# Performance work log

Measured on AMD Instinct MI355X. Metric: run time of the kernel, lower is better.

## Reference

```python
import jax, jax.numpy as jnp
import numpy as np

N, E = 50000, 300000
IN_C, HID, OUT_C, HEADS = 256, 64, 128, 4
HW = HID * HEADS  # 256


def gat_conv(x, edge_index, W, att_src, att_dst, bias, concat):
    # x: [N, F_in], W: [F_in, H*C], att_*: [H, C], edge_index: [2, E] (src -> dst)
    H, C = att_src.shape
    n = x.shape[0]
    src, dst = edge_index[0], edge_index[1]
    h = (x @ W).reshape(n, H, C)                      # [N, H, C]
    a_src = jnp.einsum('nhc,hc->nh', h, att_src)      # [N, H]
    a_dst = jnp.einsum('nhc,hc->nh', h, att_dst)      # [N, H]
    e = jax.nn.leaky_relu(a_src[src] + a_dst[dst], 0.2)  # [E, H]
    m = jax.ops.segment_max(e, dst, num_segments=n)   # per-dst max for stable softmax
    m = jnp.where(jnp.isfinite(m), m, 0.0)
    ex = jnp.exp(e - m[dst])                          # [E, H]
    denom = jax.ops.segment_sum(ex, dst, num_segments=n)
    alpha = ex / (denom[dst] + 1e-16)                 # [E, H]
    msg = h[src] * alpha[:, :, None]                  # [E, H, C]
    out = jax.ops.segment_sum(msg, dst, num_segments=n)  # [N, H, C]
    if concat:
        return out.reshape(n, H * C) + bias
    return out.mean(axis=1) + bias


def setup_inputs() -> dict:
    key = jax.random.key(0)
    ks = jax.random.split(key, 24)
    inp = {}
    inp['x'] = jax.random.normal(ks[0], (N, IN_C), dtype=jnp.float32)
    inp['edge_index'] = jax.random.randint(ks[1], (2, E), 0, N, dtype=jnp.int32)
    def glorot(k, shape):
        fan = shape[0] + shape[-1]
        return jax.random.uniform(k, shape, jnp.float32, -1.0, 1.0) * np.sqrt(6.0 / fan)
    # layer 0: GATConv(256 -> 64, heads=4, concat) + Linear(256 -> 256)
    inp['W0'] = glorot(ks[2], (IN_C, HW)); inp['as0'] = glorot(ks[3], (HEADS, HID)); inp['ad0'] = glorot(ks[4], (HEADS, HID)); inp['b0'] = jnp.zeros((HW,), jnp.float32)
    inp['lw0'] = glorot(ks[5], (IN_C, HW)); inp['lb0'] = jnp.zeros((HW,), jnp.float32)
    # layer 1: GATConv(256 -> 64, heads=4, concat) + Linear(256 -> 256)
    inp['W1'] = glorot(ks[6], (HW, HW)); inp['as1'] = glorot(ks[7], (HEADS, HID)); inp['ad1'] = glorot(ks[8], (HEADS, HID)); inp['b1'] = jnp.zeros((HW,), jnp.float32)
    inp['lw1'] = glorot(ks[9], (HW, HW)); inp['lb1'] = jnp.zeros((HW,), jnp.float32)
    # layer 2: GATConv(256 -> 128, heads=4, concat=False mean) + Linear(256 -> 128)
    inp['W2'] = glorot(ks[10], (HW, HEADS * OUT_C)); inp['as2'] = glorot(ks[11], (HEADS, OUT_C)); inp['ad2'] = glorot(ks[12], (HEADS, OUT_C)); inp['b2'] = jnp.zeros((OUT_C,), jnp.float32)
    inp['lw2'] = glorot(ks[13], (HW, OUT_C)); inp['lb2'] = jnp.zeros((OUT_C,), jnp.float32)
    return inp


def reference(x, edge_index, W0, as0, ad0, b0, lw0, lb0, W1, as1, ad1, b1, lw1, lb1, W2, as2, ad2, b2, lw2, lb2):
    # layer 0
    h = gat_conv(x, edge_index, W0, as0, ad0, b0, concat=True) + (x @ lw0 + lb0)
    h = jax.nn.elu(h)  # dropout p=0.0 -> identity
    # layer 1
    h = gat_conv(h, edge_index, W1, as1, ad1, b1, concat=True) + (h @ lw1 + lb1)
    h = jax.nn.elu(h)
    # layer 2 (no activation)
    out = gat_conv(h, edge_index, W2, as2, ad2, b2, concat=False) + (h @ lw2 + lb2)
    return out
```

## Files before the change

### kernel.cpp

```cpp
#include <hip/hip_runtime.h>
#include <cstddef>


typedef __bf16 bf16x8 __attribute__((ext_vector_type(8)));
typedef float floatx4 __attribute__((ext_vector_type(4)));
typedef unsigned short ushortx8 __attribute__((ext_vector_type(8)));

__device__ __forceinline__ unsigned short bf16_rn(float f) {
    unsigned int u = __float_as_uint(f);
    u += 0x7FFF + ((u >> 16) & 1);
    return (unsigned short)(u >> 16);
}
__device__ __forceinline__ float bf16_tof(unsigned short h) {
    return __uint_as_float(((unsigned int)h) << 16);
}

__device__ __forceinline__ float amax_decode(unsigned int u) {
    unsigned int bits = (u >> 31) ? (u & 0x7FFFFFFFu) : ~u;
    return __uint_as_float(bits);
}

__device__ __forceinline__ void gload_lds16(const void* g, void* l) {
    __builtin_amdgcn_global_load_lds(
        (const __attribute__((address_space(1))) unsigned int*)g,
        (__attribute__((address_space(3))) unsigned int*)l, 16, 0, 0);
}


__global__ __launch_bounds__(1024) void scan_kernel(const int* __restrict__ deg,
                                                    int* __restrict__ off, int n) {
    __shared__ int wsum[16];
    __shared__ int carry_s;
    int tid = threadIdx.x, lane = tid & 63, wid = tid >> 6;
    if (tid == 0) { carry_s = 0; off[0] = 0; }
    __syncthreads();
    for (int base = 0; base < n; base += 1024) {
        int i = base + tid;
        int v = (i < n) ? deg[i] : 0;
        int s = v;
        #pragma unroll
        for (int d = 1; d < 64; d <<= 1) {
            int t = __shfl_up(s, d, 64);
            if (lane >= d) s += t;
        }
        if (lane == 63) wsum[wid] = s;
        __syncthreads();
        if (wid == 0) {
            int wv = (lane < 16) ? wsum[lane] : 0;
            #pragma unroll
            for (int d = 1; d < 16; d <<= 1) {
                int t = __shfl_up(wv, d, 64);
                if (lane >= d) wv += t;
            }
            if (lane < 16) wsum[lane] = wv;
        }
        __syncthreads();
        int prev = (wid > 0) ? wsum[wid - 1] : 0;
        int inc = carry_s + prev + s;
        if (i < n) off[i + 1] = inc;
        int chunk_total = wsum[15];
        __syncthreads();
        if (tid == 0) carry_s += chunk_total;
        __syncthreads();
    }
}


__global__ __launch_bounds__(256) void wprep_kernel(
    const float* __restrict__ W0, const float* __restrict__ lw0,
    const float* __restrict__ W1, const float* __restrict__ lw1,
    const float* __restrict__ W2, const float* __restrict__ lw2,
    ushort* __restrict__ B0h, ushort* __restrict__ B0l,
    ushort* __restrict__ B1h, ushort* __restrict__ B1l,
    ushort* __restrict__ B2h, ushort* __restrict__ B2l,
    const float* __restrict__ as0, const float* __restrict__ ad0,
    const float* __restrict__ as1, const float* __restrict__ ad1,
    const float* __restrict__ as2, const float* __restrict__ ad2,
    float* __restrict__ vsd0, float* __restrict__ vsd1, float* __restrict__ vsd2,
    const int* __restrict__ edst, int* __restrict__ deg, int E)
{
    int bid = blockIdx.x, tid = threadIdx.x;
    if (bid < 1664) {
        const float* src; ushort* dh; ushort* dl; int Ncols, roff, base;
        if (bid < 256)       { src = W0;  dh = B0h; dl = B0l; Ncols = 256; roff = 0;   base = 0; }
        else if (bid < 512)  { src = lw0; dh = B0h; dl = B0l; Ncols = 256; roff = 256; base = 256; }
        else if (bid < 768)  { src = W1;  dh = B1h; dl = B1l; Ncols = 256; roff = 0;   base = 512; }
        else if (bid < 1024) { src = lw1; dh = B1h; dl = B1l; Ncols = 256; roff = 256; base = 768; }
        else if (bid < 1536) { src = W2;  dh = B2h; dl = B2l; Ncols = 512; roff = 0;   base = 1024; }
        else                 { src = lw2; dh = B2h; dl = B2l; Ncols = 128; roff = 512; base = 1536; }
        int idx = (bid - base) * 256 + tid;
        int k = idx / Ncols, n = idx - k * Ncols;
        float v = src[idx];
        unsigned short hi = bf16_rn(v);
        unsigned short lo = bf16_rn(v - bf16_tof(hi));
        int row = n + roff;
        int poff = ((row >> 4) * 8 + (k >> 5)) * 512 + (((row & 15) + 16 * ((k & 31) >> 3)) << 3) + (k & 7);
        dh[poff] = hi;
        dl[poff] = lo;
    } else if (bid < 1676) {
        int fj = (bid - 1664) >> 2;
        int idx = ((bid - 1664) & 3) * 256 + tid;
        const float *W, *as_, *ad_; float* vsd; int C;
        if (fj == 0)      { W = W0; as_ = as0; ad_ = ad0; vsd = vsd0; C = 64; }
        else if (fj == 1) { W = W1; as_ = as1; ad_ = ad1; vsd = vsd1; C = 64; }
        else              { W = W2; as_ = as2; ad_ = ad2; vsd = vsd2; C = 128; }
        int k = idx >> 2, hh = idx & 3;
        const float* wp = W + (size_t)k * (4 * C) + hh * C;
        float s = 0.f, d = 0.f;
        for (int c = 0; c < C; c++) {
            float w = wp[c];
            s += w * as_[hh * C + c];
            d += w * ad_[hh * C + c];
        }
        vsd[k * 8 + hh] = s;
        vsd[k * 8 + 4 + hh] = d;
    } else {
        int e = (bid - 1676) * 256 + tid;
        if (e < E) atomicAdd(&deg[edst[e]], 1);
    }
}


__global__ __launch_bounds__(256, 6) void scatter_split_kernel(
    const int* __restrict__ esrc, const int* __restrict__ edst,
    const int* __restrict__ off, int* __restrict__ cursor,
    int* __restrict__ csrc, int E, int egrid,
    const float* __restrict__ x, const float* __restrict__ vsd,
    ushort* __restrict__ Aph, ushort* __restrict__ Apl,
    float* __restrict__ asrc, float* __restrict__ adst, int n)
{
    int bid = blockIdx.x;
    if (bid < egrid) {
        int e = bid * 256 + threadIdx.x;
        if (e < E) {
            int d = edst[e];
            int p = off[d] + atomicAdd(&cursor[d], 1);
            csrc[p] = esrc[e];
        }
        return;
    }
    int sb = bid - egrid;
    int wid = threadIdx.x >> 6, lane = threadIdx.x & 63;
    int half = lane >> 5, sl = lane & 31;
    int d = sb * 8 + wid * 2 + half;
    if (d >= n) return;
    int k0 = sl * 8;
    float4 va = *(const float4*)(x + (size_t)d * 256 + k0);
    float4 vb = *(const float4*)(x + (size_t)d * 256 + k0 + 4);
    float v[8] = {va.x, va.y, va.z, va.w, vb.x, vb.y, vb.z, vb.w};

    ushortx8 hi, lo;
    #pragma unroll
    for (int j = 0; j < 8; ++j) {
        unsigned short h8 = bf16_rn(v[j]);
        hi[j] = h8;
        lo[j] = bf16_rn(v[j] - bf16_tof(h8));
    }
    int poff = ((d >> 4) * 8 + (k0 >> 5)) * 512 + (((d & 15) + 16 * ((k0 & 31) >> 3)) << 3);
    *(ushortx8*)(Aph + poff) = hi;
    *(ushortx8*)(Apl + poff) = lo;

    const float* vp = vsd + (size_t)k0 * 8;
    float pa[4] = {0.f, 0.f, 0.f, 0.f}, pb[4] = {0.f, 0.f, 0.f, 0.f};
    #pragma unroll
    for (int r = 0; r < 8; ++r) {
        float4 ra = *(const float4*)(vp + r * 8);
        float4 rb = *(const float4*)(vp + r * 8 + 4);
        pa[0] += v[r] * ra.x; pa[1] += v[r] * ra.y;
        pa[2] += v[r] * ra.z; pa[3] += v[r] * ra.w;
        pb[0] += v[r] * rb.x; pb[1] += v[r] * rb.y;
        pb[2] += v[r] * rb.z; pb[3] += v[r] * rb.w;
    }
    #pragma unroll
    for (int o = 1; o < 32; o <<= 1) {
        #pragma unroll
        for (int j = 0; j < 4; ++j) {
            pa[j] += __shfl_xor(pa[j], o, 64);
            pb[j] += __shfl_xor(pb[j], o, 64);
        }
    }
    if (sl == 0) {
        *(float4*)(asrc + (size_t)d * 4) = make_float4(pa[0], pa[1], pa[2], pa[3]);
        *(float4*)(adst + (size_t)d * 4) = make_float4(pb[0], pb[1], pb[2], pb[3]);
    }
}

__global__ __launch_bounds__(256) void amax_kernel(const float* __restrict__ asrc,
                                                   unsigned int* __restrict__ amax, int n) {
    int tid = threadIdx.x;
    float4 m4 = make_float4(-1e30f, -1e30f, -1e30f, -1e30f);
    for (int i = blockIdx.x * 256 + tid; i < n; i += gridDim.x * 256) {
        float4 v = ((const float4*)asrc)[i];
        m4.x = fmaxf(m4.x, v.x); m4.y = fmaxf(m4.y, v.y);
        m4.z = fmaxf(m4.z, v.z); m4.w = fmaxf(m4.w, v.w);
    }
    #pragma unroll
    for (int o = 32; o > 0; o >>= 1) {
        m4.x = fmaxf(m4.x, __shfl_down(m4.x, o, 64));
        m4.y = fmaxf(m4.y, __shfl_down(m4.y, o, 64));
        m4.z = fmaxf(m4.z, __shfl_down(m4.z, o, 64));
        m4.w = fmaxf(m4.w, __shfl_down(m4.w, o, 64));
    }
    __shared__ float sm[4][4];
    int wid = tid >> 6, lane = tid & 63;
    if (lane == 0) { sm[wid][0] = m4.x; sm[wid][1] = m4.y; sm[wid][2] = m4.z; sm[wid][3] = m4.w; }
    __syncthreads();
    if (tid < 4) {
        float v = fmaxf(fmaxf(sm[0][tid], sm[1][tid]), fmaxf(sm[2][tid], sm[3][tid]));
        unsigned int u = __float_as_uint(v);
        u = (u >> 31) ? ~u : (u | 0x80000000u);
        atomicMax(&amax[tid], u);
    }
}


__global__ __launch_bounds__(256, 2) void gemm_mfma_kernel(
    const ushort* __restrict__ Aph, const ushort* __restrict__ Apl,
    const ushort* __restrict__ Bph, const ushort* __restrict__ Bpl,
    ushort* __restrict__ O1, int n1, ushort* __restrict__ O2,
    const float* __restrict__ bias2,
    int gm, int M, int N)
{
    __shared__ __align__(16) char smem[65536];
    int gy = N >> 7;
    int bid = blockIdx.x;
    int k8 = bid & 7, sb = bid >> 3;
    int ny = sb % gy, bxi = sb / gy;
    int bx = bxi * 8 + k8;
    if (bx >= gm) return;
    int bm = bx * 128, bn = ny * 128;

    int tid = threadIdx.x, lane = tid & 63, wv = tid >> 6;
    int wm = (wv >> 1) * 64, wn = (wv & 1) * 64;
    int fr = lane & 15, q = lane >> 4;

    const ushort* sp;
    size_t gbase;
    if (wv == 0)      { sp = Aph; gbase = (size_t)(bm >> 4) * 4096; }
    else if (wv == 1) { sp = Apl; gbase = (size_t)(bm >> 4) * 4096; }
    else if (wv == 2) { sp = Bph; gbase = (size_t)(bn >> 4) * 4096; }
    else              { sp = Bpl; gbase = (size_t)(bn >> 4) * 4096; }
    size_t gsrc = gbase + (size_t)lane * 8;
    int lbase = wv * 8192;

    int agl = (wv >> 1) * 4;
    int bgl = (wv & 1) * 4;

    floatx4 acc[4][4] = {};

    #pragma unroll
    for (int t = 0; t < 8; ++t)
        gload_lds16(sp + gsrc + (size_t)t * 4096, smem + lbase + t * 1024);
    __syncthreads();

    #pragma unroll
    for (int it = 0; it < 8; ++it) {
        int cur = (it & 1) << 15;
        if (it < 7) {
            int nb = ((it + 1) & 1) << 15;
            size_t co = gsrc + (size_t)(it + 1) * 512;
            #pragma unroll
            for (int t = 0; t < 8; ++t)
                gload_lds16(sp + co + (size_t)t * 4096, smem + nb + lbase + t * 1024);
        }
        bf16x8 cah[4], cal[4], cbh[4], cbl[4];
        #pragma unroll
        for (int i = 0; i < 4; ++i) {
            cah[i] = *(const bf16x8*)(smem + cur + (agl + i) * 1024 + lane * 16);
            cal[i] = *(const bf16x8*)(smem + cur + 8192 + (agl + i) * 1024 + lane * 16);
            cbh[i] = *(const bf16x8*)(smem + cur + 16384 + (bgl + i) * 1024 + lane * 16);
            cbl[i] = *(const bf16x8*)(smem + cur + 24576 + (bgl + i) * 1024 + lane * 16);
        }
        #pragma unroll
        for (int i = 0; i < 4; ++i)
            #pragma unroll
            for (int j = 0; j < 4; ++j) {
                acc[i][j] = __builtin_amdgcn_mfma_f32_16x16x32_bf16(cah[i], cbh[j], acc[i][j], 0, 0, 0);
                acc[i][j] = __builtin_amdgcn_mfma_f32_16x16x32_bf16(cah[i], cbl[j], acc[i][j], 0, 0, 0);
                acc[i][j] = __builtin_amdgcn_mfma_f32_16x16x32_bf16(cal[i], cbh[j], acc[i][j], 0, 0, 0);
            }
        if (it < 7) __syncthreads();
    }

    int n2 = N - n1;
    #pragma unroll
    for (int i = 0; i < 4; ++i) {
        #pragma unroll
        for (int r = 0; r < 4; ++r) {
            int grow = bm + wm + i * 16 + q * 4 + r;
            if (grow < M) {
                #pragma unroll
                for (int j = 0; j < 4; ++j) {
                    int gcol = bn + wn + j * 16 + fr;
                    float v = acc[i][j][r];
                    if (gcol < n1) {
                        O1[(size_t)grow * n1 + gcol] = bf16_rn(v);
                    } else {
                        v += bias2[gcol - n1];
                        O2[(size_t)grow * n2 + (gcol - n1)] = bf16_rn(v);
                    }
                }
            }
        }
    }
}


__global__ __launch_bounds__(256, 6) void agg01_kernel(
    const ushort* __restrict__ h,
    const float* __restrict__ asrc, const float* __restrict__ adst,
    const unsigned int* __restrict__ amax,
    const int* __restrict__ off, const int* __restrict__ csrc,
    const ushort* __restrict__ lin,
    const float* __restrict__ bias,
    ushort* __restrict__ Aph, ushort* __restrict__ Apl,
    const float* __restrict__ vsd_next,
    float* __restrict__ asrc_out, float* __restrict__ adst_out,
    int n)
{
    int wid = threadIdx.x >> 6, lane = threadIdx.x & 63;
    int half = lane >> 5, sl = lane & 31;
    int d = blockIdx.x * 8 + wid * 2 + half;
    bool valid = (d < n);
    int dd = valid ? d : (n - 1);
    int head = sl >> 3;
    int c0 = sl * 8;
    float a_d = adst[dd * 4 + head];
    float mh = amax_decode(amax[head]) + a_d;
    float m = (mh > 0.f) ? mh : 0.2f * mh;
    int s0 = off[dd], s1 = valid ? off[dd + 1] : s0;
    int s1e = s1 - 1;

    float denom = 0.f;
    float ac[8] = {0.f, 0.f, 0.f, 0.f, 0.f, 0.f, 0.f, 0.f};
    for (int i = s0; i < s1; i += 4) {
        int i1 = (i + 1 < s1) ? i + 1 : s1e;
        int i2 = (i + 2 < s1) ? i + 2 : s1e;
        int i3 = (i + 3 < s1) ? i + 3 : s1e;
        int sa = csrc[i], sb = csrc[i1], sc = csrc[i2], sd = csrc[i3];
        float ea = asrc[sa * 4 + head];
        float eb = asrc[sb * 4 + head];
        float ec = asrc[sc * 4 + head];
        float ed = asrc[sd * 4 + head];
        ushortx8 hva = *(const ushortx8*)(h + (size_t)sa * 256 + c0);
        ushortx8 hvb = *(const ushortx8*)(h + (size_t)sb * 256 + c0);
        ushortx8 hvc = *(const ushortx8*)(h + (size_t)sc * 256 + c0);
        ushortx8 hvd = *(const ushortx8*)(h + (size_t)sd * 256 + c0);
        ea += a_d; ea = (ea > 0.f) ? ea : 0.2f * ea; float wa = __expf(ea - m);
        eb += a_d; eb = (eb > 0.f) ? eb : 0.2f * eb; float wb = __expf(eb - m);
        ec += a_d; ec = (ec > 0.f) ? ec : 0.2f * ec; float wc = __expf(ec - m);
        ed += a_d; ed = (ed > 0.f) ? ed : 0.2f * ed; float wd = __expf(ed - m);
        wb = (i + 1 < s1) ? wb : 0.f;
        wc = (i + 2 < s1) ? wc : 0.f;
        wd = (i + 3 < s1) ? wd : 0.f;
        denom += wa;
        #pragma unroll
        for (int j = 0; j < 8; ++j) ac[j] += wa * bf16_tof(hva[j]);
        denom += wb;
        #pragma unroll
        for (int j = 0; j < 8; ++j) ac[j] += wb * bf16_tof(hvb[j]);
        denom += wc;
        #pragma unroll
        for (int j = 0; j < 8; ++j) ac[j] += wc * bf16_tof(hvc[j]);
        denom += wd;
        #pragma unroll
        for (int j = 0; j < 8; ++j) ac[j] += wd * bf16_tof(hvd[j]);
    }

    if (valid) {
        float inv = 1.f / (denom + 1e-16f);
        float4 b4a = *(const float4*)(bias + c0);
        float4 b4b = *(const float4*)(bias + c0 + 4);
        ushortx8 l8 = *(const ushortx8*)(lin + (size_t)dd * 256 + c0);
        float v[8];
        v[0] = ac[0] * inv + b4a.x + bf16_tof(l8[0]);
        v[1] = ac[1] * inv + b4a.y + bf16_tof(l8[1]);
        v[2] = ac[2] * inv + b4a.z + bf16_tof(l8[2]);
        v[3] = ac[3] * inv + b4a.w + bf16_tof(l8[3]);
        v[4] = ac[4] * inv + b4b.x + bf16_tof(l8[4]);
        v[5] = ac[5] * inv + b4b.y + bf16_tof(l8[5]);
        v[6] = ac[6] * inv + b4b.z + bf16_tof(l8[6]);
        v[7] = ac[7] * inv + b4b.w + bf16_tof(l8[7]);
        #pragma unroll
        for (int j = 0; j < 8; ++j)
            v[j] = (v[j] > 0.f) ? v[j] : (__expf(v[j]) - 1.f);

        ushortx8 oh, ol;
        #pragma unroll
        for (int j = 0; j < 8; ++j) {
            unsigned short hi = bf16_rn(v[j]);
            oh[j] = hi;
            ol[j] = bf16_rn(v[j] - bf16_tof(hi));
        }
        int poff = ((dd >> 4) * 8 + (c0 >> 5)) * 512 + (((dd & 15) + 16 * ((c0 & 31) >> 3)) << 3);
        *(ushortx8*)(Aph + poff) = oh;
        *(ushortx8*)(Apl + poff) = ol;

        const float* vp = vsd_next + (size_t)c0 * 8;
        float pa[4] = {0.f, 0.f, 0.f, 0.f}, pb[4] = {0.f, 0.f, 0.f, 0.f};
        #pragma unroll
        for (int r = 0; r < 8; ++r) {
            float4 ra = *(const float4*)(vp + r * 8);
            float4 rb = *(const float4*)(vp + r * 8 + 4);
            pa[0] += v[r] * ra.x; pa[1] += v[r] * ra.y;
            pa[2] += v[r] * ra.z; pa[3] += v[r] * ra.w;
            pb[0] += v[r] * rb.x; pb[1] += v[r] * rb.y;
            pb[2] += v[r] * rb.z; pb[3] += v[r] * rb.w;
        }
        #pragma unroll
        for (int o = 1; o < 32; o <<= 1) {
            #pragma unroll
            for (int j = 0; j < 4; ++j) {
                pa[j] += __shfl_xor(pa[j], o, 64);
                pb[j] += __shfl_xor(pb[j], o, 64);
            }
        }
        if (sl == 0) {
            *(float4*)(asrc_out + (size_t)dd * 4) = make_float4(pa[0], pa[1], pa[2], pa[3]);
            *(float4*)(adst_out + (size_t)dd * 4) = make_float4(pb[0], pb[1], pb[2], pb[3]);
        }
    }
}


__global__ __launch_bounds__(256, 6) void agg2_kernel(
    const ushort* __restrict__ h,
    const float* __restrict__ asrc, const float* __restrict__ adst,
    const unsigned int* __restrict__ amax,
    const int* __restrict__ off, const int* __restrict__ csrc,
    const ushort* __restrict__ lin,
    const float* __restrict__ bias,
    float* __restrict__ out,
    int n)
{
    int wid = threadIdx.x >> 6, lane = threadIdx.x & 63;
    int d = blockIdx.x * 4 + wid;
    if (d >= n) return;
    int ha = lane >> 5;
    int hb = ha + 2;
    int c0 = lane * 4;
    float ad_a = adst[d * 4 + ha];
    float ad_b = adst[d * 4 + hb];
    float mha = amax_decode(amax[ha]) + ad_a;
    float mhb = amax_decode(amax[hb]) + ad_b;
    float ma = (mha > 0.f) ? mha : 0.2f * mha;
    float mb = (mhb > 0.f) ? mhb : 0.2f * mhb;
    int s0 = off[d], s1 = off[d + 1];
    int s1e = s1 - 1;

    float da = 0.f, db = 0.f;
    floatx4 aa = {0.f, 0.f, 0.f, 0.f}, ab = {0.f, 0.f, 0.f, 0.f};
    for (int i = s0; i < s1; i += 4) {
        int i1 = (i + 1 < s1) ? i + 1 : s1e;
        int i2 = (i + 2 < s1) ? i + 2 : s1e;
        int i3 = (i + 3 < s1) ? i + 3 : s1e;
        int sw = csrc[i], sx = csrc[i1], sy = csrc[i2], sz = csrc[i3];
        float ea0 = asrc[sw * 4 + ha], eb0 = asrc[sw * 4 + hb];
        float ea1 = asrc[sx * 4 + ha], eb1 = asrc[sx * 4 + hb];
        float ea2 = asrc[sy * 4 + ha], eb2 = asrc[sy * 4 + hb];
        float ea3 = asrc[sz * 4 + ha], eb3 = asrc[sz * 4 + hb];
        ushort4 va0 = *(const ushort4*)(h + (size_t)sw * 512 + c0);
        ushort4 vb0 = *(const ushort4*)(h + (size_t)sw * 512 + 256 + c0);
        ushort4 va1 = *(const ushort4*)(h + (size_t)sx * 512 + c0);
        ushort4 vb1 = *(const ushort4*)(h + (size_t)sx * 512 + 256 + c0);
        ushort4 va2 = *(const ushort4*)(h + (size_t)sy * 512 + c0);
        ushort4 vb2 = *(const ushort4*)(h + (size_t)sy * 512 + 256 + c0);
        ushort4 va3 = *(const ushort4*)(h + (size_t)sz * 512 + c0);
        ushort4 vb3 = *(const ushort4*)(h + (size_t)sz * 512 + 256 + c0);
        ea0 += ad_a; ea0 = (ea0 > 0.f) ? ea0 : 0.2f * ea0; float wa0 = __expf(ea0 - ma);
        eb0 += ad_b; eb0 = (eb0 > 0.f) ? eb0 : 0.2f * eb0; float wb0 = __expf(eb0 - mb);
        ea1 += ad_a; ea1 = (ea1 > 0.f) ? ea1 : 0.2f * ea1; float wa1 = __expf(ea1 - ma);
        eb1 += ad_b; eb1 = (eb1 > 0.f) ? eb1 : 0.2f * eb1; float wb1 = __expf(eb1 - mb);
        ea2 += ad_a; ea2 = (ea2 > 0.f) ? ea2 : 0.2f * ea2; float wa2 = __expf(ea2 - ma);
        eb2 += ad_b; eb2 = (eb2 > 0.f) ? eb2 : 0.2f * eb2; float wb2 = __expf(eb2 - mb);
        ea3 += ad_a; ea3 = (ea3 > 0.f) ? ea3 : 0.2f * ea3; float wa3 = __expf(ea3 - ma);
        eb3 += ad_b; eb3 = (eb3 > 0.f) ? eb3 : 0.2f * eb3; float wb3 = __expf(eb3 - mb);
        wa1 = (i + 1 < s1) ? wa1 : 0.f;  wb1 = (i + 1 < s1) ? wb1 : 0.f;
        wa2 = (i + 2 < s1) ? wa2 : 0.f;  wb2 = (i + 2 < s1) ? wb2 : 0.f;
        wa3 = (i + 3 < s1) ? wa3 : 0.f;  wb3 = (i + 3 < s1) ? wb3 : 0.f;
        da += wa0; db += wb0;
        aa[0] += wa0 * bf16_tof(va0.x); aa[1] += wa0 * bf16_tof(va0.y);
        aa[2] += wa0 * bf16_tof(va0.z); aa[3] += wa0 * bf16_tof(va0.w);
        ab[0] += wb0 * bf16_tof(vb0.x); ab[1] += wb0 * bf16_tof(vb0.y);
        ab[2] += wb0 * bf16_tof(vb0.z); ab[3] += wb0 * bf16_tof(vb0.w);
        da += wa1; db += wb1;
        aa[0] += wa1 * bf16_tof(va1.x); aa[1] += wa1 * bf16_tof(va1.y);
        aa[2] += wa1 * bf16_tof(va1.z); aa[3] += wa1 * bf16_tof(va1.w);
        ab[0] += wb1 * bf16_tof(vb1.x); ab[1] += wb1 * bf16_tof(vb1.y);
        ab[2] += wb1 * bf16_tof(vb1.z); ab[3] += wb1 * bf16_tof(vb1.w);
        da += wa2; db += wb2;
        aa[0] += wa2 * bf16_tof(va2.x); aa[1] += wa2 * bf16_tof(va2.y);
        aa[2] += wa2 * bf16_tof(va2.z); aa[3] += wa2 * bf16_tof(va2.w);
        ab[0] += wb2 * bf16_tof(vb2.x); ab[1] += wb2 * bf16_tof(vb2.y);
        ab[2] += wb2 * bf16_tof(vb2.z); ab[3] += wb2 * bf16_tof(vb2.w);
        da += wa3; db += wb3;
        aa[0] += wa3 * bf16_tof(va3.x); aa[1] += wa3 * bf16_tof(va3.y);
        aa[2] += wa3 * bf16_tof(va3.z); aa[3] += wa3 * bf16_tof(va3.w);
        ab[0] += wb3 * bf16_tof(vb3.x); ab[1] += wb3 * bf16_tof(vb3.y);
        ab[2] += wb3 * bf16_tof(vb3.z); ab[3] += wb3 * bf16_tof(vb3.w);
    }
    float ia = 1.f / (da + 1e-16f), ib = 1.f / (db + 1e-16f);
    float s4[4];
    #pragma unroll
    for (int j = 0; j < 4; ++j) s4[j] = aa[j] * ia + ab[j] * ib;
    float p4[4];
    #pragma unroll
    for (int j = 0; j < 4; ++j) p4[j] = __shfl_xor(s4[j], 32, 64);
    if (lane < 32) {
        float4 b4 = *(const float4*)(bias + c0);
        ushort4 l4 = *(const ushort4*)(lin + (size_t)d * 128 + c0);
        float4 o;
        o.x = 0.25f * (s4[0] + p4[0]) + b4.x + bf16_tof(l4.x);
        o.y = 0.25f * (s4[1] + p4[1]) + b4.y + bf16_tof(l4.y);
        o.z = 0.25f * (s4[2] + p4[2]) + b4.z + bf16_tof(l4.z);
        o.w = 0.25f * (s4[3] + p4[3]) + b4.w + bf16_tof(l4.w);
        *(float4*)(out + (size_t)d * 128 + c0) = o;
    }
}


extern "C" void kernel_launch(void* const* d_in, const int* in_sizes, int n_in,
                              void* d_out, int out_size, void* d_ws, size_t ws_size,
                              hipStream_t stream)
{
    const float* x   = (const float*)d_in[0];
    const int*   ei  = (const int*)d_in[1];
    const float* W0  = (const float*)d_in[2];
    const float* as0 = (const float*)d_in[3];
    const float* ad0 = (const float*)d_in[4];
    const float* b0  = (const float*)d_in[5];
    const float* lw0 = (const float*)d_in[6];
    const float* lb0 = (const float*)d_in[7];
    const float* W1  = (const float*)d_in[8];
    const float* as1 = (const float*)d_in[9];
    const float* ad1 = (const float*)d_in[10];
    const float* b1  = (const float*)d_in[11];
    const float* lw1 = (const float*)d_in[12];
    const float* lb1 = (const float*)d_in[13];
    const float* W2  = (const float*)d_in[14];
    const float* as2 = (const float*)d_in[15];
    const float* ad2 = (const float*)d_in[16];
    const float* b2  = (const float*)d_in[17];
    const float* lw2 = (const float*)d_in[18];
    const float* lb2 = (const float*)d_in[19];
    float* out = (float*)d_out;

    const int N = in_sizes[0] / 256;
    const int E = in_sizes[1] / 2;
    const int* esrc = ei;
    const int* edst = ei + E;

    const int gm = (N + 127) / 128;
    const int gmp = ((gm + 7) / 8) * 8;
    const size_t Agroups = (size_t)gm * 8;

    char* p = (char*)d_ws;
    ushort* act_hi = (ushort*)p; p += Agroups * 8 * 512 * 2;
    ushort* act_lo = (ushort*)p; p += Agroups * 8 * 512 * 2;
    ushort* h      = (ushort*)p; p += (size_t)N * 512 * 2;
    ushort* lin    = (ushort*)p; p += (size_t)N * 256 * 2;
    float*  as_a   = (float*)p;  p += (size_t)N * 4 * 4;
    float*  ad_a   = (float*)p;  p += (size_t)N * 4 * 4;
    float*  as_b   = (float*)p;  p += (size_t)N * 4 * 4;
    float*  ad_b   = (float*)p;  p += (size_t)N * 4 * 4;
    ushort* B0h = (ushort*)p; p += (size_t)32 * 8 * 512 * 2;
    ushort* B0l = (ushort*)p; p += (size_t)32 * 8 * 512 * 2;
    ushort* B1h = (ushort*)p; p += (size_t)32 * 8 * 512 * 2;
    ushort* B1l = (ushort*)p; p += (size_t)32 * 8 * 512 * 2;
    ushort* B2h = (ushort*)p; p += (size_t)40 * 8 * 512 * 2;
    ushort* B2l = (ushort*)p; p += (size_t)40 * 8 * 512 * 2;
    float* vsd0 = (float*)p; p += 256 * 8 * 4;
    float* vsd1 = (float*)p; p += 256 * 8 * 4;
    float* vsd2 = (float*)p; p += 256 * 8 * 4;
    unsigned int* amax = (unsigned int*)p;
    int* deg    = (int*)(amax + 12);
    int* off    = deg + N;
    int* cursor = off + N + 1;
    int* csrc   = cursor + N;

    hipMemsetAsync(amax, 0, sizeof(int) * (size_t)(3 * N + 13), stream);

    int egrid = (E + 255) / 256;
    int g4 = (N + 3) / 4;
    int g8 = (N + 7) / 8;

    wprep_kernel<<<1676 + egrid, 256, 0, stream>>>(W0, lw0, W1, lw1, W2, lw2,
                                                   B0h, B0l, B1h, B1l, B2h, B2l,
                                                   as0, ad0, as1, ad1, as2, ad2,
                                                   vsd0, vsd1, vsd2,
                                                   edst, deg, E);
    scan_kernel<<<1, 1024, 0, stream>>>(deg, off, N);

    scatter_split_kernel<<<egrid + g8, 256, 0, stream>>>(esrc, edst, off, cursor, csrc, E, egrid,
                                                         x, vsd0, act_hi, act_lo, as_a, ad_a, N);
    amax_kernel<<<32, 256, 0, stream>>>(as_a, amax + 0, N);

    gemm_mfma_kernel<<<gmp * 4, 256, 0, stream>>>(act_hi, act_lo, B0h, B0l, h, 256, lin, lb0, gm, N, 512);
    agg01_kernel<<<g8, 256, 0, stream>>>(h, as_a, ad_a, amax + 0, off, csrc, lin, b0,
                                         act_hi, act_lo, vsd1, as_b, ad_b, N);
    amax_kernel<<<32, 256, 0, stream>>>(as_b, amax + 4, N);

    gemm_mfma_kernel<<<gmp * 4, 256, 0, stream>>>(act_hi, act_lo, B1h, B1l, h, 256, lin, lb1, gm, N, 512);
    agg01_kernel<<<g8, 256, 0, stream>>>(h, as_b, ad_b, amax + 4, off, csrc, lin, b1,
                                         act_hi, act_lo, vsd2, as_a, ad_a, N);
    amax_kernel<<<32, 256, 0, stream>>>(as_a, amax + 8, N);

    gemm_mfma_kernel<<<gmp * 5, 256, 0, stream>>>(act_hi, act_lo, B2h, B2l, h, 512, lin, lb2, gm, N, 640);
    agg2_kernel<<<g4, 256, 0, stream>>>(h, as_a, ad_a, amax + 8, off, csrc, lin, b2, out, N);
}
```

Before: 678.6 us.

## Split GEMM K-step into hi and lo phases to halve LDS buffer

The split-bf16 MFMA GEMM now streams the high and low halves of each K-slice as separate pipeline phases. This halves shared memory to 32KB so more blocks can be resident per CU, and keeps the high fragments in registers for the following low phase. The cost is twice as many barrier-separated phases, each with less MFMA work to hide the load latency behind.

```diff
diff --git a/kernel.cpp b/kernel.cpp
--- a/kernel.cpp
+++ b/kernel.cpp
@@ -221,7 +221,7 @@
     const float* __restrict__ bias2,
     int gm, int M, int N)
 {
-    __shared__ __align__(16) char smem[65536];
+    __shared__ __align__(16) char smem[32768];
     int gy = N >> 7;
     int bid = blockIdx.x;
     int k8 = bid & 7, sb = bid >> 3;
@@ -234,52 +234,61 @@
     int wm = (wv >> 1) * 64, wn = (wv & 1) * 64;
     int fr = lane & 15, q = lane >> 4;
 
-    const ushort* sp;
-    size_t gbase;
-    if (wv == 0)      { sp = Aph; gbase = (size_t)(bm >> 4) * 4096; }
-    else if (wv == 1) { sp = Apl; gbase = (size_t)(bm >> 4) * 4096; }
-    else if (wv == 2) { sp = Bph; gbase = (size_t)(bn >> 4) * 4096; }
-    else              { sp = Bpl; gbase = (size_t)(bn >> 4) * 4096; }
-    size_t gsrc = gbase + (size_t)lane * 8;
-    int lbase = wv * 8192;
+    const ushort* sp_h = (wv < 2) ? Aph : Bph;
+    const ushort* sp_l = (wv < 2) ? Apl : Bpl;
+    size_t gsrc = ((size_t)((wv < 2) ? (bm >> 4) : (bn >> 4)) + (size_t)((wv & 1) * 4)) * 4096
+                + (size_t)lane * 8;
+    int lbase = wv * 4096;
 
     int agl = (wv >> 1) * 4;
     int bgl = (wv & 1) * 4;
 
     floatx4 acc[4][4] = {};
-
-    #pragma unroll
-    for (int t = 0; t < 8; ++t)
-        gload_lds16(sp + gsrc + (size_t)t * 4096, smem + lbase + t * 1024);
+    bf16x8 cah[4], cbh[4];
+
+    #pragma unroll
+    for (int t = 0; t < 4; ++t)
+        gload_lds16(sp_h + gsrc + (size_t)t * 4096, smem + lbase + t * 1024);
     __syncthreads();
 
     #pragma unroll
-    for (int it = 0; it < 8; ++it) {
-        int cur = (it & 1) << 15;
-        if (it < 7) {
-            int nb = ((it + 1) & 1) << 15;
-            size_t co = gsrc + (size_t)(it + 1) * 512;
+    for (int p = 0; p < 16; ++p) {
+        int cur = (p & 1) << 14;
+        if (p < 15) {
+            int nb = ((p + 1) & 1) << 14;
+            const ushort* sp = ((p + 1) & 1) ? sp_l : sp_h;
+            size_t co = gsrc + (size_t)((p + 1) >> 1) * 512;
             #pragma unroll
-            for (int t = 0; t < 8; ++t)
+            for (int t = 0; t < 4; ++t)
                 gload_lds16(sp + co + (size_t)t * 4096, smem + nb + lbase + t * 1024);
         }
-        bf16x8 cah[4], cal[4], cbh[4], cbl[4];
-        #pragma unroll
-        for (int i = 0; i < 4; ++i) {
-            cah[i] = *(const bf16x8*)(smem + cur + (agl + i) * 1024 + lane * 16);
-            cal[i] = *(const bf16x8*)(smem + cur + 8192 + (agl + i) * 1024 + lane * 16);
-            cbh[i] = *(const bf16x8*)(smem + cur + 16384 + (bgl + i) * 1024 + lane * 16);
-            cbl[i] = *(const bf16x8*)(smem + cur + 24576 + (bgl + i) * 1024 + lane * 16);
-        }
-        #pragma unroll
-        for (int i = 0; i < 4; ++i)
+        if (!(p & 1)) {
             #pragma unroll
-            for (int j = 0; j < 4; ++j) {
-                acc[i][j] = __builtin_amdgcn_mfma_f32_16x16x32_bf16(cah[i], cbh[j], acc[i][j], 0, 0, 0);
-                acc[i][j] = __builtin_amdgcn_mfma_f32_16x16x32_bf16(cah[i], cbl[j], acc[i][j], 0, 0, 0);
-                acc[i][j] = __builtin_amdgcn_mfma_f32_16x16x32_bf16(cal[i], cbh[j], acc[i][j], 0, 0, 0);
+            for (int i = 0; i < 4; ++i) {
+                cah[i] = *(const bf16x8*)(smem + cur + (agl + i) * 1024 + lane * 16);
+                cbh[i] = *(const bf16x8*)(smem + cur + 8192 + (bgl + i) * 1024 + lane * 16);
             }
-        if (it < 7) __syncthreads();
+            #pragma unroll
+            for (int i = 0; i < 4; ++i)
+                #pragma unroll
+                for (int j = 0; j < 4; ++j)
+                    acc[i][j] = __builtin_amdgcn_mfma_f32_16x16x32_bf16(cah[i], cbh[j], acc[i][j], 0, 0, 0);
+        } else {
+            bf16x8 cal[4], cbl[4];
+            #pragma unroll
+            for (int i = 0; i < 4; ++i) {
+                cal[i] = *(const bf16x8*)(smem + cur + (agl + i) * 1024 + lane * 16);
+                cbl[i] = *(const bf16x8*)(smem + cur + 8192 + (bgl + i) * 1024 + lane * 16);
+            }
+            #pragma unroll
+            for (int i = 0; i < 4; ++i)
+                #pragma unroll
+                for (int j = 0; j < 4; ++j) {
+                    acc[i][j] = __builtin_amdgcn_mfma_f32_16x16x32_bf16(cah[i], cbl[j], acc[i][j], 0, 0, 0);
+                    acc[i][j] = __builtin_amdgcn_mfma_f32_16x16x32_bf16(cal[i], cbh[j], acc[i][j], 0, 0, 0);
+                }
+        }
+        if (p < 15) __syncthreads();
     }
 
     int n2 = N - n1;
```

Result: faster. 641.4 us (-5.5%).
